# Kernel optimization log

Measured on AMD Instinct MI355X. Metric: run time of the kernel, lower is better.

Reference implementation:

```python
import jax, jax.numpy as jnp
import numpy as np

RADIUS = (0.1, 0.1, 0.1)  # radius_x, radius_y, radius_z (cube half-widths)
NSAMPLE = 32


def setup_inputs() -> dict:
    key = jax.random.key(0)
    k1, k2, k3 = jax.random.split(key, 3)
    B, Nb, Mb, C = 4, 16384, 4096, 64
    xyz = jax.random.uniform(k1, (B * Nb, 3), dtype=jnp.float32)
    new_xyz = jax.random.uniform(k2, (B * Mb, 3), dtype=jnp.float32)
    features = jax.random.normal(k3, (B * Nb, C), dtype=jnp.float32)
    xyz_batch_cnt = jnp.full((B,), Nb, dtype=jnp.int32)
    new_xyz_batch_cnt = jnp.full((B,), Mb, dtype=jnp.int32)
    return {
        "xyz": xyz,
        "xyz_batch_cnt": xyz_batch_cnt,
        "new_xyz": new_xyz,
        "new_xyz_batch_cnt": new_xyz_batch_cnt,
        "features": features,
    }


def _cube_query(xyz_b, new_b, rx, ry, rz, nsample):
    # xyz_b: (B, Nb, 3); new_b: (B, Mb, 3)
    Nb = xyz_b.shape[1]

    def per_batch(args):
        pts, qs = args  # (Nb,3), (Mb,3)
        # cube membership test per axis (avoid stacking a (Mb,Nb,3) tensor)
        mask = (
            (jnp.abs(qs[:, None, 0] - pts[None, :, 0]) < rx)
            & (jnp.abs(qs[:, None, 1] - pts[None, :, 1]) < ry)
            & (jnp.abs(qs[:, None, 2] - pts[None, :, 2]) < rz)
        )  # (Mb, Nb)
        # CUDA kernel keeps the FIRST nsample neighbors in point order:
        # score favors in-cube points, tie-broken by smallest index.
        score = jnp.where(mask, -jnp.arange(Nb, dtype=jnp.float32), -jnp.inf)
        vals, idx_local = jax.lax.top_k(score, nsample)  # (Mb, nsample)
        valid = jnp.isfinite(vals)  # non_padding
        return idx_local, valid

    # process one batch at a time to bound the MbxNb intermediate
    idx_l, valid = jax.lax.map(per_batch, (xyz_b, new_b))
    return idx_l, valid


def reference(xyz, xyz_batch_cnt, new_xyz, new_xyz_batch_cnt, features):
    rx, ry, rz = RADIUS
    nsample = NSAMPLE
    B = xyz_batch_cnt.shape[0]
    N, M = xyz.shape[0], new_xyz.shape[0]
    Nb, Mb = N // B, M // B  # equal counts per batch (matches setup_inputs)

    xyz_b = xyz.reshape(B, Nb, 3)
    new_b = new_xyz.reshape(B, Mb, 3)

    idx_l, valid = _cube_query(xyz_b, new_b, rx, ry, rz, nsample)
    # local -> global flattened indices (batch offsets)
    offsets = (jnp.arange(B, dtype=idx_l.dtype) * Nb)[:, None, None]
    idx = (idx_l + offsets).reshape(M, nsample)
    valid = valid.reshape(M, nsample)
    # torch zeroes idx for empty/padding slots before gather
    idx = jnp.where(valid, idx, 0)

    non_padding = valid.astype(features.dtype)  # (M, nsample)
    grouped = features[idx]  # (M, nsample, C) gather
    # empty_ball_mask + padding_mask zeroing, fused into one multiply
    grouped = grouped * non_padding[..., None]
    grouped = jnp.transpose(grouped, (0, 2, 1))  # (M, C, nsample)
    num_non_padding = jnp.sum(non_padding, axis=-1)  # (M,)
    return grouped, num_non_padding
```

## Files before the change

### kernel.cpp

```cpp
#include <hip/hip_runtime.h>

#define NSAMPLE 32
#define RADI 0.1f
#define WPB 4
#define MARGIN 0.0002f

#define NCELL 4
#define NBLKA 3
#define SPAN  2
#define NBLK3 27
#define CAP   3072
#define NSEG  64
#define NXCD  8

typedef float nat_f32x4 __attribute__((ext_vector_type(4)));

__device__ __forceinline__ int cell_of(float x) {
    int c = (int)(x * (float)NCELL);
    c = c < 0 ? 0 : c;
    return c > (NCELL - 1) ? (NCELL - 1) : c;
}

__global__ __launch_bounds__(64 * WPB) void count_kernel(
    const float* __restrict__ xyz, const int* __restrict__ xyz_cnt,
    int* __restrict__ segcnt, int B)
{
    const int wave = threadIdx.x >> 6, lane = threadIdx.x & 63;
    const int gw = blockIdx.x * WPB + wave;
    if (gw >= B * NBLK3 * NSEG) return;
    const int seg = gw % NSEG;
    const int blk = (gw / NSEG) % NBLK3;
    const int b   = gw / (NSEG * NBLK3);
    const int bx = blk % NBLKA, by = (blk / NBLKA) % NBLKA, bz = blk / (NBLKA * NBLKA);

    int xstart = 0;
    for (int i = 0; i < b; ++i) xstart += xyz_cnt[i];
    const int nb = xyz_cnt[b];
    const int seglen = (nb + NSEG - 1) / NSEG;
    const int p0 = seg * seglen;
    const int p1 = min(p0 + seglen, nb);

    const float* __restrict__ xp = xyz + (size_t)xstart * 3;

    int cnt = 0;
    for (int base = p0; base < p1; base += 256) {
        #pragma unroll
        for (int k = 0; k < 4; ++k) {
            const int p = base + k * 64 + lane;
            bool hit = false;
            if (p < p1) {
                const float x = xp[p * 3 + 0];
                const float y = xp[p * 3 + 1];
                const float z = xp[p * 3 + 2];
                hit = ((unsigned)(cell_of(x) - bx) < (unsigned)SPAN) &
                      ((unsigned)(cell_of(y) - by) < (unsigned)SPAN) &
                      ((unsigned)(cell_of(z) - bz) < (unsigned)SPAN);
            }
            cnt += (int)__popcll(__ballot(hit));
        }
    }
    if (lane == 0) segcnt[gw] = cnt;
}

__global__ __launch_bounds__(64 * WPB) void fill_kernel(
    const float* __restrict__ xyz, const int* __restrict__ xyz_cnt,
    const int* __restrict__ segcnt, float4* __restrict__ blk_pts,
    int* __restrict__ blkcnt, int B)
{
    const int wave = threadIdx.x >> 6, lane = threadIdx.x & 63;
    const int gw = blockIdx.x * WPB + wave;
    if (gw >= B * NBLK3 * NSEG) return;
    const int seg = gw % NSEG;
    const int blk = (gw / NSEG) % NBLK3;
    const int b   = gw / (NSEG * NBLK3);
    const int bx = blk % NBLKA, by = (blk / NBLKA) % NBLKA, bz = blk / (NBLKA * NBLKA);

    int xstart = 0;
    for (int i = 0; i < b; ++i) xstart += xyz_cnt[i];
    const int nb = xyz_cnt[b];
    const int seglen = (nb + NSEG - 1) / NSEG;
    const int p0 = seg * seglen;
    const int p1 = min(p0 + seglen, nb);

    const int bid = b * NBLK3 + blk;
    int off = 0;
    const int sbase = bid * NSEG;
    for (int s = 0; s < seg; ++s) off += segcnt[sbase + s];

    const float* __restrict__ xp = xyz + (size_t)xstart * 3;
    float4* __restrict__ dst = blk_pts + (size_t)bid * CAP;
    const unsigned long long lt = (1ull << lane) - 1ull;

    int cnt = 0;
    for (int base = p0; base < p1; base += 256) {
        #pragma unroll
        for (int k = 0; k < 4; ++k) {
            const int p = base + k * 64 + lane;
            bool hit = false;
            float x = 0.f, y = 0.f, z = 0.f;
            if (p < p1) {
                x = xp[p * 3 + 0];
                y = xp[p * 3 + 1];
                z = xp[p * 3 + 2];
                hit = ((unsigned)(cell_of(x) - bx) < (unsigned)SPAN) &
                      ((unsigned)(cell_of(y) - by) < (unsigned)SPAN) &
                      ((unsigned)(cell_of(z) - bz) < (unsigned)SPAN);
            }
            const unsigned long long m = __ballot(hit);
            if (hit) {
                const int slot = off + cnt + (int)__popcll(m & lt);
                if (slot < CAP) {
                    float4 v;
                    v.x = x; v.y = y; v.z = z;
                    v.w = __int_as_float(xstart + p);
                    dst[slot] = v;
                }
            }
            cnt += (int)__popcll(m);
        }
    }
    if (seg == NSEG - 1 && lane == 0) blkcnt[bid] = off + cnt;
}

__global__ __launch_bounds__(64 * WPB, 8) void query_kernel(
    const float4* __restrict__ blk_pts,
    const int*    __restrict__ blkcnt,
    const float*  __restrict__ new_xyz,
    const int*    __restrict__ new_cnt,
    const float*  __restrict__ features,
    float* __restrict__ out_grouped,
    float* __restrict__ out_cnt,
    int B, int M, int C)
{
    const int wave = threadIdx.x >> 6;
    const int lane = threadIdx.x & 63;

    int lbid;
    {
        const int nwg = (int)gridDim.x;
        const int qq = nwg / NXCD, rr = nwg % NXCD;
        const int xcd = (int)blockIdx.x % NXCD;
        const int base = (xcd < rr) ? xcd * (qq + 1) : rr * (qq + 1) + (xcd - rr) * qq;
        lbid = base + (int)blockIdx.x / NXCD;
    }
    const int q = lbid * WPB + wave;
    if (q >= M) return;

    __shared__ int s_idx_all[WPB][NSAMPLE];
    int* __restrict__ s_idx = s_idx_all[wave];
    if (lane < NSAMPLE) s_idx[lane] = 0;

    int b = 0, qacc = 0;
    for (int i = 0; i < B; ++i) {
        const int qc = new_cnt[i];
        if (q < qacc + qc) { b = i; break; }
        qacc += qc;
    }

    const float qx = new_xyz[q * 3 + 0];
    const float qy = new_xyz[q * 3 + 1];
    const float qz = new_xyz[q * 3 + 2];

    const int bxq = min(max((int)floorf((qx - RADI - MARGIN) * (float)NCELL), 0), NBLKA - 1);
    const int byq = min(max((int)floorf((qy - RADI - MARGIN) * (float)NCELL), 0), NBLKA - 1);
    const int bzq = min(max((int)floorf((qz - RADI - MARGIN) * (float)NCELL), 0), NBLKA - 1);
    const int bid = b * NBLK3 + bxq + NBLKA * byq + NBLKA * NBLKA * bzq;

    const float4* __restrict__ lp = blk_pts + (size_t)bid * CAP;

    float4 A[4], Bb[4];
    #pragma unroll
    for (int k = 0; k < 4; ++k) A[k] = lp[k * 64 + lane];
    #pragma unroll
    for (int k = 0; k < 4; ++k) Bb[k] = lp[256 + k * 64 + lane];
    int lcnt = blkcnt[bid];
    if (lcnt > CAP) lcnt = CAP;

    const unsigned long long lt = (1ull << lane) - 1ull;
    int found = 0, base = 0;
    const int nfull = lcnt & ~255;

    auto test_group = [&](const float4& v, bool inb) {
        const float m3 = fmaxf(fmaxf(fabsf(qx - v.x), fabsf(qy - v.y)),
                               fabsf(qz - v.z));
        const bool c = inb & (m3 < RADI);
        const unsigned long long m = __ballot(c);
        if (c) {
            const int slot = found + (int)__popcll(m & lt);
            if (slot < NSAMPLE) s_idx[slot] = __float_as_int(v.w);
        }
        found += (int)__popcll(m);
    };

    if (nfull > 0) {
        while (true) {
            #pragma unroll
            for (int k = 0; k < 4; ++k) {
                test_group(A[k], true);
                if (found >= NSAMPLE) break;
            }
            base += 256;
            if (found >= NSAMPLE || base >= nfull) break;

            if (base + 256 < nfull) {
                #pragma unroll
                for (int k = 0; k < 4; ++k) A[k] = lp[base + 256 + k * 64 + lane];
            }
            #pragma unroll
            for (int k = 0; k < 4; ++k) {
                test_group(Bb[k], true);
                if (found >= NSAMPLE) break;
            }
            base += 256;
            if (found >= NSAMPLE || base >= nfull) break;

            if (base + 256 < nfull) {
                #pragma unroll
                for (int k = 0; k < 4; ++k) Bb[k] = lp[base + 256 + k * 64 + lane];
            }
        }
    }
    while (found < NSAMPLE && base < lcnt) {
        #pragma unroll
        for (int k = 0; k < 4; ++k) {
            const int p = base + k * 64 + lane;
            const bool inb = (p < lcnt);
            const float4 v = lp[inb ? p : 0];
            test_group(v, inb);
        }
        base += 256;
    }
    if (found > NSAMPLE) found = NSAMPLE;

    asm volatile("s_waitcnt lgkmcnt(0)" ::: "memory");
    __builtin_amdgcn_sched_barrier(0);

    const int s0  = 4 * (lane & 7);
    const int chi = lane >> 3;
    const int r0 = s_idx[s0 + 0];
    const int r1 = s_idx[s0 + 1];
    const int r2 = s_idx[s0 + 2];
    const int r3 = s_idx[s0 + 3];
    const float k0 = (s0 + 0) < found ? 1.0f : 0.0f;
    const float k1 = (s0 + 1) < found ? 1.0f : 0.0f;
    const float k2 = (s0 + 2) < found ? 1.0f : 0.0f;
    const float k3 = (s0 + 3) < found ? 1.0f : 0.0f;

    const float* __restrict__ f0p = features + (size_t)r0 * C;
    const float* __restrict__ f1p = features + (size_t)r1 * C;
    const float* __restrict__ f2p = features + (size_t)r2 * C;
    const float* __restrict__ f3p = features + (size_t)r3 * C;

    float* __restrict__ og = out_grouped + (size_t)q * (C * NSAMPLE);
    #pragma unroll
    for (int k = 0; k < 8; ++k) {
        const int c = 8 * k + chi;
        nat_f32x4 v;
        v.x = f0p[c] * k0;
        v.y = f1p[c] * k1;
        v.z = f2p[c] * k2;
        v.w = f3p[c] * k3;
        __builtin_nontemporal_store(v,
            reinterpret_cast<nat_f32x4*>(og + (size_t)(k * 64 + lane) * 4));
    }
    if (lane == 0) out_cnt[q] = (float)found;
}

__global__ __launch_bounds__(64 * WPB, 8) void fallback_kernel(
    const float* __restrict__ xyz, const int* __restrict__ xyz_cnt,
    const float* __restrict__ new_xyz, const int* __restrict__ new_cnt,
    const float* __restrict__ features,
    float* __restrict__ out_grouped, float* __restrict__ out_cnt,
    int B, int M, int C)
{
    const int wave = threadIdx.x >> 6, lane = threadIdx.x & 63;
    const int q = blockIdx.x * WPB + wave;
    if (q >= M) return;

    __shared__ int s_idx_all[WPB][NSAMPLE];
    int* __restrict__ s_idx = s_idx_all[wave];
    if (lane < NSAMPLE) s_idx[lane] = 0;

    int b = 0, qacc = 0, xstart = 0;
    for (int i = 0; i < B; ++i) {
        const int qc = new_cnt[i];
        if (q < qacc + qc) { b = i; break; }
        qacc += qc; xstart += xyz_cnt[i];
    }
    const int nb = xyz_cnt[b];
    const float qx = new_xyz[q * 3 + 0], qy = new_xyz[q * 3 + 1], qz = new_xyz[q * 3 + 2];
    const float* __restrict__ xp = xyz + (size_t)xstart * 3;
    const unsigned long long lt = (1ull << lane) - 1ull;

    int found = 0;
    for (int base = 0; base < nb && found < NSAMPLE; base += 64) {
        const int p = base + lane;
        bool c = false;
        if (p < nb) {
            const float dx = qx - xp[p * 3 + 0];
            const float dy = qy - xp[p * 3 + 1];
            const float dz = qz - xp[p * 3 + 2];
            c = (fabsf(dx) < RADI) && (fabsf(dy) < RADI) && (fabsf(dz) < RADI);
        }
        const unsigned long long m = __ballot(c);
        if (c) {
            const int slot = found + (int)__popcll(m & lt);
            if (slot < NSAMPLE) s_idx[slot] = xstart + p;
        }
        found += (int)__popcll(m);
    }
    if (found > NSAMPLE) found = NSAMPLE;

    asm volatile("s_waitcnt lgkmcnt(0)" ::: "memory");
    __builtin_amdgcn_sched_barrier(0);

    const int s0 = 4 * (lane & 7), chi = lane >> 3;
    const int r0 = s_idx[s0 + 0], r1 = s_idx[s0 + 1], r2 = s_idx[s0 + 2], r3 = s_idx[s0 + 3];
    const float k0 = (s0 + 0) < found ? 1.0f : 0.0f;
    const float k1 = (s0 + 1) < found ? 1.0f : 0.0f;
    const float k2 = (s0 + 2) < found ? 1.0f : 0.0f;
    const float k3 = (s0 + 3) < found ? 1.0f : 0.0f;
    const float* f0p = features + (size_t)r0 * C;
    const float* f1p = features + (size_t)r1 * C;
    const float* f2p = features + (size_t)r2 * C;
    const float* f3p = features + (size_t)r3 * C;
    float* __restrict__ og = out_grouped + (size_t)q * (C * NSAMPLE);
    #pragma unroll
    for (int k = 0; k < 8; ++k) {
        const int c = 8 * k + chi;
        float4 v;
        v.x = f0p[c] * k0; v.y = f1p[c] * k1; v.z = f2p[c] * k2; v.w = f3p[c] * k3;
        *reinterpret_cast<float4*>(og + (size_t)(k * 64 + lane) * 4) = v;
    }
    if (lane == 0) out_cnt[q] = (float)found;
}

extern "C" void kernel_launch(void* const* d_in, const int* in_sizes, int n_in,
                              void* d_out, int out_size, void* d_ws, size_t ws_size,
                              hipStream_t stream) {
    const float* xyz      = (const float*)d_in[0];
    const int*   xyz_cnt  = (const int*)d_in[1];
    const float* new_xyz  = (const float*)d_in[2];
    const int*   new_cnt  = (const int*)d_in[3];
    const float* features = (const float*)d_in[4];

    const int B = in_sizes[1];
    const int N = in_sizes[0] / 3;
    const int M = in_sizes[2] / 3;
    const int C = in_sizes[4] / N;

    float* out_grouped = (float*)d_out;
    float* out_cnt     = (float*)d_out + (size_t)M * C * NSAMPLE;

    const size_t blk_bytes  = (size_t)B * NBLK3 * CAP * sizeof(float4);
    const size_t seg_bytes  = (size_t)B * NBLK3 * NSEG * sizeof(int);
    const size_t bcn_bytes  = (size_t)B * NBLK3 * sizeof(int);
    const size_t need = blk_bytes + seg_bytes + bcn_bytes;

    if (ws_size >= need) {
        char* w = (char*)d_ws;
        float4* blk_pts = (float4*)w;                       w += blk_bytes;
        int*    segcnt  = (int*)w;                          w += seg_bytes;
        int*    blkcnt  = (int*)w;

        const int nbw = B * NBLK3 * NSEG;
        hipLaunchKernelGGL(count_kernel, dim3((nbw + WPB - 1) / WPB), dim3(64 * WPB), 0, stream,
                           xyz, xyz_cnt, segcnt, B);
        hipLaunchKernelGGL(fill_kernel, dim3((nbw + WPB - 1) / WPB), dim3(64 * WPB), 0, stream,
                           xyz, xyz_cnt, segcnt, blk_pts, blkcnt, B);
        hipLaunchKernelGGL(query_kernel, dim3((M + WPB - 1) / WPB), dim3(64 * WPB), 0, stream,
                           blk_pts, blkcnt, new_xyz, new_cnt, features,
                           out_grouped, out_cnt, B, M, C);
    } else {
        hipLaunchKernelGGL(fallback_kernel, dim3((M + WPB - 1) / WPB), dim3(64 * WPB), 0, stream,
                           xyz, xyz_cnt, new_xyz, new_cnt, features,
                           out_grouped, out_cnt, B, M, C);
    }
}
```

Measured before the change: 66.32 us.

## Process two queries per wavefront, prefetching the second query's points during the first epilogue

Each wavefront now handles two consecutive query points. The second query's first 512 candidate points are loaded before the first query's feature gather and store, so the scan latency of one query overlaps the epilogue of the other. The grid is halved to match. This gives fewer, longer-lived waves and so less parallelism and occupancy-based latency hiding, and adds register pressure from holding both queries' state.

```diff
diff --git a/kernel.cpp b/kernel.cpp
--- a/kernel.cpp
+++ b/kernel.cpp
@@ -143,127 +143,156 @@
         const int base = (xcd < rr) ? xcd * (qq + 1) : rr * (qq + 1) + (xcd - rr) * qq;
         lbid = base + (int)blockIdx.x / NXCD;
     }
-    const int q = lbid * WPB + wave;
-    if (q >= M) return;
-
-    __shared__ int s_idx_all[WPB][NSAMPLE];
-    int* __restrict__ s_idx = s_idx_all[wave];
-    if (lane < NSAMPLE) s_idx[lane] = 0;
-
-    int b = 0, qacc = 0;
-    for (int i = 0; i < B; ++i) {
-        const int qc = new_cnt[i];
-        if (q < qacc + qc) { b = i; break; }
-        qacc += qc;
-    }
-
-    const float qx = new_xyz[q * 3 + 0];
-    const float qy = new_xyz[q * 3 + 1];
-    const float qz = new_xyz[q * 3 + 2];
-
-    const int bxq = min(max((int)floorf((qx - RADI - MARGIN) * (float)NCELL), 0), NBLKA - 1);
-    const int byq = min(max((int)floorf((qy - RADI - MARGIN) * (float)NCELL), 0), NBLKA - 1);
-    const int bzq = min(max((int)floorf((qz - RADI - MARGIN) * (float)NCELL), 0), NBLKA - 1);
-    const int bid = b * NBLK3 + bxq + NBLKA * byq + NBLKA * NBLKA * bzq;
-
-    const float4* __restrict__ lp = blk_pts + (size_t)bid * CAP;
+    const int q0 = (lbid * WPB + wave) * 2;
+    if (q0 >= M) return;
+    const int q1 = q0 + 1;
+    const bool has1 = q1 < M;
+
+    __shared__ int s_idx_all[WPB][2][NSAMPLE];
+    int* __restrict__ sp0 = s_idx_all[wave][0];
+    int* __restrict__ sp1 = s_idx_all[wave][1];
+    (&s_idx_all[wave][0][0])[lane] = 0;
+
+    const unsigned long long lt = (1ull << lane) - 1ull;
+    const int s0  = 4 * (lane & 7);
+    const int chi = lane >> 3;
+
+    auto locate = [&](int q, float& qx, float& qy, float& qz) -> int {
+        int b = 0, qacc = 0;
+        for (int i = 0; i < B; ++i) {
+            const int qc = new_cnt[i];
+            if (q < qacc + qc) { b = i; break; }
+            qacc += qc;
+        }
+        qx = new_xyz[q * 3 + 0];
+        qy = new_xyz[q * 3 + 1];
+        qz = new_xyz[q * 3 + 2];
+        const int bx = min(max((int)floorf((qx - RADI - MARGIN) * (float)NCELL), 0), NBLKA - 1);
+        const int by = min(max((int)floorf((qy - RADI - MARGIN) * (float)NCELL), 0), NBLKA - 1);
+        const int bz = min(max((int)floorf((qz - RADI - MARGIN) * (float)NCELL), 0), NBLKA - 1);
+        return b * NBLK3 + bx + NBLKA * by + NBLKA * NBLKA * bz;
+    };
+
+    float qx0, qy0, qz0, qx1 = 0.f, qy1 = 0.f, qz1 = 0.f;
+    const int bid0 = locate(q0, qx0, qy0, qz0);
+    const int bid1 = has1 ? locate(q1, qx1, qy1, qz1) : bid0;
+    const float4* __restrict__ lp0 = blk_pts + (size_t)bid0 * CAP;
+    const float4* __restrict__ lp1 = blk_pts + (size_t)bid1 * CAP;
+    int lcnt0 = blkcnt[bid0]; if (lcnt0 > CAP) lcnt0 = CAP;
+    int lcnt1 = has1 ? blkcnt[bid1] : 0; if (lcnt1 > CAP) lcnt1 = CAP;
 
     float4 A[4], Bb[4];
-    #pragma unroll
-    for (int k = 0; k < 4; ++k) A[k] = lp[k * 64 + lane];
-    #pragma unroll
-    for (int k = 0; k < 4; ++k) Bb[k] = lp[256 + k * 64 + lane];
-    int lcnt = blkcnt[bid];
-    if (lcnt > CAP) lcnt = CAP;
-
-    const unsigned long long lt = (1ull << lane) - 1ull;
-    int found = 0, base = 0;
-    const int nfull = lcnt & ~255;
-
-    auto test_group = [&](const float4& v, bool inb) {
-        const float m3 = fmaxf(fmaxf(fabsf(qx - v.x), fabsf(qy - v.y)),
-                               fabsf(qz - v.z));
-        const bool c = inb & (m3 < RADI);
-        const unsigned long long m = __ballot(c);
-        if (c) {
-            const int slot = found + (int)__popcll(m & lt);
-            if (slot < NSAMPLE) s_idx[slot] = __float_as_int(v.w);
-        }
-        found += (int)__popcll(m);
-    };
-
-    if (nfull > 0) {
-        while (true) {
+
+    auto scan = [&](const float4* __restrict__ lp, int lcnt, int* __restrict__ sp,
+                    float qx, float qy, float qz) -> int {
+        int found = 0, base = 0;
+        const int nfull = lcnt & ~255;
+
+        auto test_group = [&](const float4& v, bool inb) {
+            const float m3 = fmaxf(fmaxf(fabsf(qx - v.x), fabsf(qy - v.y)),
+                                   fabsf(qz - v.z));
+            const bool c = inb & (m3 < RADI);
+            const unsigned long long m = __ballot(c);
+            if (c) {
+                const int slot = found + (int)__popcll(m & lt);
+                if (slot < NSAMPLE) sp[slot] = __float_as_int(v.w);
+            }
+            found += (int)__popcll(m);
+        };
+
+        if (nfull > 0) {
+            while (true) {
+                #pragma unroll
+                for (int k = 0; k < 4; ++k) {
+                    test_group(A[k], true);
+                    if (found >= NSAMPLE) break;
+                }
+                base += 256;
+                if (found >= NSAMPLE || base >= nfull) break;
+
+                if (base + 256 < nfull) {
+                    #pragma unroll
+                    for (int k = 0; k < 4; ++k) A[k] = lp[base + 256 + k * 64 + lane];
+                }
+                #pragma unroll
+                for (int k = 0; k < 4; ++k) {
+                    test_group(Bb[k], true);
+                    if (found >= NSAMPLE) break;
+                }
+                base += 256;
+                if (found >= NSAMPLE || base >= nfull) break;
+
+                if (base + 256 < nfull) {
+                    #pragma unroll
+                    for (int k = 0; k < 4; ++k) Bb[k] = lp[base + 256 + k * 64 + lane];
+                }
+            }
+        }
+        while (found < NSAMPLE && base < lcnt) {
             #pragma unroll
             for (int k = 0; k < 4; ++k) {
-                test_group(A[k], true);
-                if (found >= NSAMPLE) break;
+                const int p = base + k * 64 + lane;
+                const bool inb = (p < lcnt);
+                const float4 v = lp[inb ? p : 0];
+                test_group(v, inb);
             }
             base += 256;
-            if (found >= NSAMPLE || base >= nfull) break;
-
-            if (base + 256 < nfull) {
-                #pragma unroll
-                for (int k = 0; k < 4; ++k) A[k] = lp[base + 256 + k * 64 + lane];
-            }
-            #pragma unroll
-            for (int k = 0; k < 4; ++k) {
-                test_group(Bb[k], true);
-                if (found >= NSAMPLE) break;
-            }
-            base += 256;
-            if (found >= NSAMPLE || base >= nfull) break;
-
-            if (base + 256 < nfull) {
-                #pragma unroll
-                for (int k = 0; k < 4; ++k) Bb[k] = lp[base + 256 + k * 64 + lane];
-            }
-        }
-    }
-    while (found < NSAMPLE && base < lcnt) {
+        }
+        return found > NSAMPLE ? NSAMPLE : found;
+    };
+
+    auto epilogue = [&](int q, const int* __restrict__ sp, int found) {
+        const int r0 = sp[s0 + 0];
+        const int r1 = sp[s0 + 1];
+        const int r2 = sp[s0 + 2];
+        const int r3 = sp[s0 + 3];
+        const float k0 = (s0 + 0) < found ? 1.0f : 0.0f;
+        const float k1 = (s0 + 1) < found ? 1.0f : 0.0f;
+        const float k2 = (s0 + 2) < found ? 1.0f : 0.0f;
+        const float k3 = (s0 + 3) < found ? 1.0f : 0.0f;
+        const float* __restrict__ f0p = features + (size_t)r0 * C;
+        const float* __restrict__ f1p = features + (size_t)r1 * C;
+        const float* __restrict__ f2p = features + (size_t)r2 * C;
+        const float* __restrict__ f3p = features + (size_t)r3 * C;
+        float* __restrict__ og = out_grouped + (size_t)q * (C * NSAMPLE);
         #pragma unroll
-        for (int k = 0; k < 4; ++k) {
-            const int p = base + k * 64 + lane;
-            const bool inb = (p < lcnt);
-            const float4 v = lp[inb ? p : 0];
-            test_group(v, inb);
-        }
-        base += 256;
-    }
-    if (found > NSAMPLE) found = NSAMPLE;
+        for (int k = 0; k < 8; ++k) {
+            const int c = 8 * k + chi;
+            nat_f32x4 v;
+            v.x = f0p[c] * k0;
+            v.y = f1p[c] * k1;
+            v.z = f2p[c] * k2;
+            v.w = f3p[c] * k3;
+            __builtin_nontemporal_store(v,
+                reinterpret_cast<nat_f32x4*>(og + (size_t)(k * 64 + lane) * 4));
+        }
+        if (lane == 0) out_cnt[q] = (float)found;
+    };
+
+    #pragma unroll
+    for (int k = 0; k < 4; ++k) A[k]  = lp0[k * 64 + lane];
+    #pragma unroll
+    for (int k = 0; k < 4; ++k) Bb[k] = lp0[256 + k * 64 + lane];
+
+    const int f0 = scan(lp0, lcnt0, sp0, qx0, qy0, qz0);
+
+    if (has1) {
+        #pragma unroll
+        for (int k = 0; k < 4; ++k) A[k]  = lp1[k * 64 + lane];
+        #pragma unroll
+        for (int k = 0; k < 4; ++k) Bb[k] = lp1[256 + k * 64 + lane];
+    }
 
     asm volatile("s_waitcnt lgkmcnt(0)" ::: "memory");
     __builtin_amdgcn_sched_barrier(0);
-
-    const int s0  = 4 * (lane & 7);
-    const int chi = lane >> 3;
-    const int r0 = s_idx[s0 + 0];
-    const int r1 = s_idx[s0 + 1];
-    const int r2 = s_idx[s0 + 2];
-    const int r3 = s_idx[s0 + 3];
-    const float k0 = (s0 + 0) < found ? 1.0f : 0.0f;
-    const float k1 = (s0 + 1) < found ? 1.0f : 0.0f;
-    const float k2 = (s0 + 2) < found ? 1.0f : 0.0f;
-    const float k3 = (s0 + 3) < found ? 1.0f : 0.0f;
-
-    const float* __restrict__ f0p = features + (size_t)r0 * C;
-    const float* __restrict__ f1p = features + (size_t)r1 * C;
-    const float* __restrict__ f2p = features + (size_t)r2 * C;
-    const float* __restrict__ f3p = features + (size_t)r3 * C;
-
-    float* __restrict__ og = out_grouped + (size_t)q * (C * NSAMPLE);
-    #pragma unroll
-    for (int k = 0; k < 8; ++k) {
-        const int c = 8 * k + chi;
-        nat_f32x4 v;
-        v.x = f0p[c] * k0;
-        v.y = f1p[c] * k1;
-        v.z = f2p[c] * k2;
-        v.w = f3p[c] * k3;
-        __builtin_nontemporal_store(v,
-            reinterpret_cast<nat_f32x4*>(og + (size_t)(k * 64 + lane) * 4));
-    }
-    if (lane == 0) out_cnt[q] = (float)found;
+    epilogue(q0, sp0, f0);
+
+    if (has1) {
+        const int f1 = scan(lp1, lcnt1, sp1, qx1, qy1, qz1);
+        asm volatile("s_waitcnt lgkmcnt(0)" ::: "memory");
+        __builtin_amdgcn_sched_barrier(0);
+        epilogue(q1, sp1, f1);
+    }
 }
 
 __global__ __launch_bounds__(64 * WPB, 8) void fallback_kernel(
@@ -368,7 +397,8 @@
                            xyz, xyz_cnt, segcnt, B);
         hipLaunchKernelGGL(fill_kernel, dim3((nbw + WPB - 1) / WPB), dim3(64 * WPB), 0, stream,
                            xyz, xyz_cnt, segcnt, blk_pts, blkcnt, B);
-        hipLaunchKernelGGL(query_kernel, dim3((M + WPB - 1) / WPB), dim3(64 * WPB), 0, stream,
+        const int pairs = (M + 1) / 2;
+        hipLaunchKernelGGL(query_kernel, dim3((pairs + WPB - 1) / WPB), dim3(64 * WPB), 0, stream,
                            blk_pts, blkcnt, new_xyz, new_cnt, features,
                            out_grouped, out_cnt, B, M, C);
     } else {
```

Result: slower. 111.9 us (+68.8%).
